# Optimization experiments

Hardware: AMD Instinct MI355X
Metric: run time of the kernel (lower is better)

Reference implementation:

```python
import jax, jax.numpy as jnp
import numpy as np

N, E, NFEAT, NHID, K, TOP_N, NCLASS = 50000, 800000, 512, 128, 4, 2, 64
ALPHA = 0.2   # LeakyReLU negative slope (config.alpha)
EPS = 1e-16   # avoid 0/0 for isolated / fully-masked nodes


def _spgat_layer(h, src, dst, a, mask, concat):
    """SpGraphAttentionLayer_2: attention over given edges, no internal W.
    h: (N, F); a: (2F,); mask: optional (E,) 0/1 edge-subset mask.
    edge_e = exp(-leakyrelu(a . [h_src; h_dst]));
    out = segsum(e * h_dst) / segsum(e)  (per target node src).
    """
    F = h.shape[1]
    s1 = h @ a[:F]                     # (N,)
    s2 = h @ a[F:]                     # (N,)
    e = jnp.exp(-jax.nn.leaky_relu(s1[src] + s2[dst], ALPHA))  # (E,)
    if mask is not None:
        e = e * mask
    rowsum = jax.ops.segment_sum(e, src, num_segments=N)              # (N,)
    hp = jax.ops.segment_sum(e[:, None] * h[dst], src, num_segments=N)  # (N,F)
    hp = hp / (rowsum[:, None] + EPS)
    return jax.nn.elu(hp) if concat else hp


def setup_inputs() -> dict:
    key = jax.random.key(0)
    ks = jax.random.split(key, 7)
    x = jax.random.normal(ks[0], (N, NFEAT), jnp.float32)
    edge = jax.random.randint(ks[1], (2, E), 0, N)
    W_ks = jax.random.normal(ks[2], (K, NFEAT, NHID), jnp.float32) * 0.05
    a_k = jax.random.normal(ks[3], (K, 2 * NHID * K), jnp.float32) * 0.05
    W_o = jax.random.normal(ks[4], (NHID * K, NCLASS), jnp.float32) * 0.05
    a_att = jax.random.normal(ks[5], (K, 2 * NHID), jnp.float32) * 0.05
    a_out = jax.random.normal(ks[6], (2 * NCLASS,), jnp.float32) * 0.05
    return {"x": x, "edge": edge, "W_ks": W_ks, "a_k": a_k,
            "W_o": W_o, "a_att": a_att, "a_out": a_out}


def reference(x, edge, W_ks, a_k, W_o, a_att, a_out):
    src, dst = edge[0], edge[1]
    # K per-factor projections; dropout is a no-op in eval mode
    h_k = jnp.einsum('nf,kfh->knh', x, W_ks)              # (K, N, H)
    h = jnp.transpose(h_k, (1, 0, 2)).reshape(N, K * NHID)  # cat(h_k, dim=1)
    # Edge-level factor routing: softmax_K( a_k @ [h_src; h_dst] ).
    # Linear score => precompute per-node halves instead of (E, 2KH) gather.
    s_src = h @ a_k[:, :K * NHID].T                       # (N, K)
    s_dst = h @ a_k[:, K * NHID:].T                       # (N, K)
    edge_att = jax.nn.softmax(s_src[src] + s_dst[dst], axis=-1)  # (E, K)
    top_att, top_idx = jax.lax.top_k(edge_att, TOP_N)     # (E, TOP_N)
    # edge e belongs to factor k iff k is among its top_n factors
    masks = (top_idx[:, :, None] == jnp.arange(K)[None, None, :]).any(1)  # (E, K)
    outs = [_spgat_layer(h_k[k], src, dst, a_att[k],
                         masks[:, k].astype(h.dtype), True) for k in range(K)]
    xo = jnp.concatenate(outs, axis=1) @ W_o              # (N, NCLASS)
    xo = jax.nn.elu(_spgat_layer(xo, src, dst, a_out, None, False))
    att_loss = jnp.mean(1.0 - jnp.sum(top_att, axis=1))
    return jax.nn.log_softmax(xo, axis=1), att_loss
```

## Files before the change

kernel.cpp:

```cpp
#include <hip/hip_runtime.h>
#include <math.h>

#define NN 50000
#define NE 800000
#define NF 512
#define NH 128
#define KF 4
#define NC 64
#define LRELU_ALPHA 0.2f
#define EPSF 1e-16f

typedef unsigned short u16;
typedef __attribute__((ext_vector_type(8))) short bf16x8;
typedef __attribute__((ext_vector_type(4))) float f32x4;

#define OFF_H      0LL
#define OFF_HP     (OFF_H + (long long)NN * NF)
#define OFF_REC    (OFF_HP + (long long)NN * NF)
#define OFF_XO0    (OFF_REC + 4LL * NE)
#define OFF_SV1    (OFF_XO0 + (long long)NN * NC)
#define OFF_SV2    (OFF_SV1 + (long long)NN * 8)
#define OFF_WOT    (OFF_SV2 + (long long)NN * 8)
#define OFF_S1O    (OFF_WOT + (long long)NN * KF)
#define OFF_S2O    (OFF_S1O + NN)
#define OFF_START  (OFF_S2O + NN)
#define OFF_CNT    (OFF_START + NN + 4)
#define OFF_CURSOR (OFF_CNT + NN)
#define OFF_ATT    (OFF_CURSOR + NN)
#define WS_FLOATS  (OFF_ATT + 2)

__device__ __forceinline__ u16 bf16_rne(float f) {
    unsigned int u = __float_as_uint(f);
    return (u16)((u + 0x7FFFu + ((u >> 16) & 1u)) >> 16);
}
__device__ __forceinline__ float bf16_f(u16 b) {
    return __uint_as_float(((unsigned int)b) << 16);
}

__device__ __forceinline__ void gload_lds16(const u16* g, u16* l) {
    __builtin_amdgcn_global_load_lds(
        (const __attribute__((address_space(1))) void*)g,
        (__attribute__((address_space(3))) void*)l, 16, 0, 0);
}

#define NSPLIT 12500
#define NCNT   ((NE + 255) / 256)
__global__ __launch_bounds__(256) void split_all(
        const float* __restrict__ x, u16* __restrict__ xhi, u16* __restrict__ xlo,
        const int* __restrict__ edge, int* __restrict__ cnt,
        const float* __restrict__ Wks, const float* __restrict__ Wo,
        u16* __restrict__ wthi, u16* __restrict__ wtlo,
        u16* __restrict__ wohi, u16* __restrict__ wolo) {
    if (blockIdx.x < NSPLIT) {
        size_t i = ((size_t)blockIdx.x * 256 + threadIdx.x) * 8;
        float4 v0 = *(const float4*)(x + i);
        float4 v1 = *(const float4*)(x + i + 4);
        float v[8] = {v0.x, v0.y, v0.z, v0.w, v1.x, v1.y, v1.z, v1.w};
        unsigned int hp[4], lp[4];
#pragma unroll
        for (int j = 0; j < 4; ++j) {
            u16 h0 = bf16_rne(v[2 * j]);
            u16 h1 = bf16_rne(v[2 * j + 1]);
            u16 l0 = bf16_rne(v[2 * j] - bf16_f(h0));
            u16 l1 = bf16_rne(v[2 * j + 1] - bf16_f(h1));
            hp[j] = (unsigned int)h0 | ((unsigned int)h1 << 16);
            lp[j] = (unsigned int)l0 | ((unsigned int)l1 << 16);
        }
        *(uint4*)(xhi + i) = make_uint4(hp[0], hp[1], hp[2], hp[3]);
        *(uint4*)(xlo + i) = make_uint4(lp[0], lp[1], lp[2], lp[3]);
    } else if (blockIdx.x < NSPLIT + NCNT) {
        int e = (blockIdx.x - NSPLIT) * 256 + threadIdx.x;
        if (e < NE) atomicAdd(&cnt[edge[e]], 1);
    } else {
        int b = blockIdx.x - NSPLIT - NCNT;
        if (b < 512) {
            int kf = b >> 7, n = b & 127;
            for (int f = threadIdx.x; f < NF; f += 256) {
                float v = Wks[(size_t)kf * (NF * NH) + (size_t)f * NH + n];
                u16 hb = bf16_rne(v);
                u16 lb = bf16_rne(v - bf16_f(hb));
                wthi[(size_t)b * NF + f] = hb;
                wtlo[(size_t)b * NF + f] = lb;
            }
        } else {
            int n = b - 512;
            for (int f = threadIdx.x; f < NF; f += 256) {
                float v = Wo[(size_t)f * NC + n];
                u16 hb = bf16_rne(v);
                u16 lb = bf16_rne(v - bf16_f(hb));
                wohi[(size_t)n * NF + f] = hb;
                wolo[(size_t)n * NF + f] = lb;
            }
        }
    }
}

__global__ __launch_bounds__(256) void gemm_h_mfma(
        const u16* __restrict__ xhi, const u16* __restrict__ xlo,
        const u16* __restrict__ wthi, const u16* __restrict__ wtlo,
        float* __restrict__ h) {
    __shared__ u16 Ah[128 * 32], Al[128 * 32], Bh[128 * 32], Bl[128 * 32];
    const int nwg = 4 * ((NN + 127) / 128);
    const int q = nwg / 8, r = nwg % 8;
    int o = blockIdx.x;
    int xcd = o & 7, pos = o >> 3;
    int wg = (xcd < r ? xcd * (q + 1) : r * (q + 1) + (xcd - r) * q) + pos;
    int m0 = (wg >> 2) * 128, n0 = (wg & 3) * 128;

    int tid = threadIdx.x;
    int lane = tid & 63;
    int wave = tid >> 6, wm = wave >> 1, wn = wave & 1;
    f32x4 acc[4][4];
#pragma unroll
    for (int i = 0; i < 4; ++i)
#pragma unroll
        for (int j = 0; j < 4; ++j) acc[i][j] = (f32x4)(0.f);

    u16* sbuf = (wave == 0) ? Ah : (wave == 1) ? Al : (wave == 2) ? Bh : Bl;
    const u16* gbase = (wave == 0) ? xhi : (wave == 1) ? xlo
                     : (wave == 2) ? wthi : wtlo;
    int rowbase = (wave < 2) ? m0 : n0;
    int c16s = (lane & 3) ^ ((lane >> 2) & 3) ^ (lane >> 4);
    const u16* gsrc[8];
#pragma unroll
    for (int i = 0; i < 8; ++i) {
        int rowg = rowbase + 16 * i + (lane >> 2);
        if (wave < 2 && rowg >= NN) rowg = NN - 1;
        gsrc[i] = gbase + (size_t)rowg * NF + c16s * 8;
    }

    const int arow = wm * 64 + (lane & 15);
    const int brow = wn * 64 + (lane & 15);
    const int rc16 = (lane >> 4) ^ ((lane & 3) ^ ((lane >> 2) & 3));
    const int fragoff = rc16 * 8;

    for (int k0 = 0; k0 < NF; k0 += 32) {
        __syncthreads();
#pragma unroll
        for (int i = 0; i < 8; ++i)
            gload_lds16(gsrc[i] + k0, sbuf + i * 512);
        __syncthreads();
        bf16x8 ah[4], al[4], bh[4], bl[4];
#pragma unroll
        for (int mi = 0; mi < 4; ++mi) {
            ah[mi] = *(const bf16x8*)(Ah + (arow + mi * 16) * 32 + fragoff);
            al[mi] = *(const bf16x8*)(Al + (arow + mi * 16) * 32 + fragoff);
        }
#pragma unroll
        for (int ni = 0; ni < 4; ++ni) {
            bh[ni] = *(const bf16x8*)(Bh + (brow + ni * 16) * 32 + fragoff);
            bl[ni] = *(const bf16x8*)(Bl + (brow + ni * 16) * 32 + fragoff);
        }
#pragma unroll
        for (int mi = 0; mi < 4; ++mi)
#pragma unroll
            for (int ni = 0; ni < 4; ++ni) {
                acc[mi][ni] = __builtin_amdgcn_mfma_f32_16x16x32_bf16(
                    ah[mi], bh[ni], acc[mi][ni], 0, 0, 0);
                acc[mi][ni] = __builtin_amdgcn_mfma_f32_16x16x32_bf16(
                    ah[mi], bl[ni], acc[mi][ni], 0, 0, 0);
                acc[mi][ni] = __builtin_amdgcn_mfma_f32_16x16x32_bf16(
                    al[mi], bh[ni], acc[mi][ni], 0, 0, 0);
            }
    }
#pragma unroll
    for (int mi = 0; mi < 4; ++mi) {
        int mbase = m0 + wm * 64 + mi * 16 + (lane >> 4) * 4;
#pragma unroll
        for (int ni = 0; ni < 4; ++ni) {
            int n = n0 + wn * 64 + ni * 16 + (lane & 15);
#pragma unroll
            for (int r2 = 0; r2 < 4; ++r2) {
                int m = mbase + r2;
                if (m < NN) h[(size_t)m * NF + n] = acc[mi][ni][r2];
            }
        }
    }
}

__global__ __launch_bounds__(256) void compute_svals_h(
        const float* __restrict__ h, const float* __restrict__ a_k,
        const float* __restrict__ a_att,
        float* __restrict__ sv1, float* __restrict__ sv2) {
    __shared__ float Ak[4][1024];
    __shared__ float Aa[4][256];
    for (int i = threadIdx.x; i < 4096; i += 256) Ak[i >> 10][i & 1023] = a_k[i];
    for (int i = threadIdx.x; i < 1024; i += 256) Aa[i >> 8][i & 255] = a_att[i];
    __syncthreads();
    int w = threadIdx.x >> 6, lane = threadIdx.x & 63;
    for (int n = blockIdx.x * 4 + w; n < NN; n += gridDim.x * 4) {
        const float* hr = h + (size_t)n * NF;
        float accS[4] = {0, 0, 0, 0}, accD[4] = {0, 0, 0, 0};
        float accQ1[4] = {0, 0, 0, 0}, accQ2[4] = {0, 0, 0, 0};
#pragma unroll
        for (int i = 0; i < 8; ++i) {
            int f = i * 64 + lane;
            float hv = hr[f];
#pragma unroll
            for (int k = 0; k < 4; ++k) {
                accS[k] = fmaf(hv, Ak[k][f], accS[k]);
                accD[k] = fmaf(hv, Ak[k][512 + f], accD[k]);
            }
            accQ1[i >> 1] = fmaf(hv, Aa[i >> 1][f & 127], accQ1[i >> 1]);
            accQ2[i >> 1] = fmaf(hv, Aa[i >> 1][128 + (f & 127)], accQ2[i >> 1]);
        }
#pragma unroll
        for (int off = 32; off >= 1; off >>= 1) {
#pragma unroll
            for (int k = 0; k < 4; ++k) {
                accS[k] += __shfl_xor(accS[k], off);
                accD[k] += __shfl_xor(accD[k], off);
                accQ1[k] += __shfl_xor(accQ1[k], off);
                accQ2[k] += __shfl_xor(accQ2[k], off);
            }
        }
        if (lane == 0) {
#pragma unroll
            for (int k = 0; k < 4; ++k) {
                sv1[(size_t)n * 8 + k]     = accS[k];
                sv1[(size_t)n * 8 + 4 + k] = accQ1[k];
                sv2[(size_t)n * 8 + k]     = accD[k];
                sv2[(size_t)n * 8 + 4 + k] = accQ2[k];
            }
        }
    }
}

__global__ __launch_bounds__(1024) void csr_scan(const int* __restrict__ cnt,
                                                 int* __restrict__ start) {
    __shared__ int part[1024];
    int t = threadIdx.x;
    const int CH = (NN + 1023) / 1024;
    int base = t * CH;
    int s = 0;
    for (int i = 0; i < CH; ++i) {
        int idx = base + i;
        if (idx < NN) s += cnt[idx];
    }
    part[t] = s;
    __syncthreads();
    for (int off = 1; off < 1024; off <<= 1) {
        int v = (t >= off) ? part[t - off] : 0;
        __syncthreads();
        part[t] += v;
        __syncthreads();
    }
    int run = (t == 0) ? 0 : part[t - 1];
    for (int i = 0; i < CH; ++i) {
        int idx = base + i;
        if (idx < NN) { start[idx] = run; run += cnt[idx]; }
    }
    if (t == 1023) start[NN] = run;
}

__global__ __launch_bounds__(256) void edge_pre1(
        const int* __restrict__ edge, const int* __restrict__ start,
        int* __restrict__ cursor,
        const float* __restrict__ sv1, const float* __restrict__ sv2,
        int4* __restrict__ rec, double* __restrict__ att_acc) {
    __shared__ float blk[4];
    int tid = threadIdx.x;
    int e = blockIdx.x * 256 + tid;
    float t2 = 0.f;
    if (e < NE) {
        int src = edge[e];
        int dst = edge[NE + e];
        const float* p1 = sv1 + (size_t)src * 8;
        const float* p2 = sv2 + (size_t)dst * 8;
        float4 ss = *(const float4*)(p1);
        float4 q1 = *(const float4*)(p1 + 4);
        float4 sd = *(const float4*)(p2);
        float4 q2 = *(const float4*)(p2 + 4);
        float l0 = ss.x + sd.x, l1 = ss.y + sd.y, l2 = ss.z + sd.z, l3 = ss.w + sd.w;
        int i1 = 0; float v1 = l0;
        if (l1 > v1) { v1 = l1; i1 = 1; }
        if (l2 > v1) { v1 = l2; i1 = 2; }
        if (l3 > v1) { v1 = l3; i1 = 3; }
        int i2 = 0; float v2 = -3.4e38f;
        if (i1 != 0)            { v2 = l0; i2 = 0; }
        if (i1 != 1 && l1 > v2) { v2 = l1; i2 = 1; }
        if (i1 != 2 && l2 > v2) { v2 = l2; i2 = 2; }
        if (i1 != 3 && l3 > v2) { v2 = l3; i2 = 3; }
        float esum = expf(l0 - v1) + expf(l1 - v1) + expf(l2 - v1) + expf(l3 - v1);
        t2 = (1.f + expf(v2 - v1)) / esum;
        float q1v1 = i1 == 0 ? q1.x : i1 == 1 ? q1.y : i1 == 2 ? q1.z : q1.w;
        float q2v1 = i1 == 0 ? q2.x : i1 == 1 ? q2.y : i1 == 2 ? q2.z : q2.w;
        float q1v2 = i2 == 0 ? q1.x : i2 == 1 ? q1.y : i2 == 2 ? q1.z : q1.w;
        float q2v2 = i2 == 0 ? q2.x : i2 == 1 ? q2.y : i2 == 2 ? q2.z : q2.w;
        float sv1v = q1v1 + q2v1, sv2v = q1v2 + q2v2;
        float ee1 = expf(-(sv1v >= 0.f ? sv1v : LRELU_ALPHA * sv1v));
        float ee2 = expf(-(sv2v >= 0.f ? sv2v : LRELU_ALPHA * sv2v));
        int p = start[src] + atomicAdd(&cursor[src], 1);
        rec[p] = make_int4(dst, src | (i1 << 16) | (i2 << 18),
                           __float_as_int(ee1), __float_as_int(ee2));
    }
#pragma unroll
    for (int off = 32; off >= 1; off >>= 1) t2 += __shfl_xor(t2, off);
    if ((tid & 63) == 0) blk[tid >> 6] = t2;
    __syncthreads();
    if (tid == 0)
        atomicAdd(att_acc, (double)(blk[0] + blk[1] + blk[2] + blk[3]));
}

#define G1_LOAD(RR, T)                                                          \
    int i1##T = __builtin_amdgcn_readfirstlane(((RR).y >> 16) & 3);             \
    int i2##T = __builtin_amdgcn_readfirstlane(((RR).y >> 18) & 3);             \
    int dd##T = __builtin_amdgcn_readfirstlane((RR).x);                         \
    float w1##T = __uint_as_float(__builtin_amdgcn_readfirstlane((RR).z));      \
    float w2##T = __uint_as_float(__builtin_amdgcn_readfirstlane((RR).w));      \
    const float* hr##T = h + (size_t)dd##T * NF + lane;                         \
    float v1a##T = hr##T[i1##T * 128];                                          \
    float v1b##T = hr##T[i1##T * 128 + 64];                                     \
    float v2a##T = hr##T[i2##T * 128];                                          \
    float v2b##T = hr##T[i2##T * 128 + 64];

#define G1_ACC(T)                                                               \
    switch (i1##T) {                                                            \
        case 0: a00 = fmaf(w1##T, v1a##T, a00); a01 = fmaf(w1##T, v1b##T, a01); rs0 += w1##T; break; \
        case 1: a10 = fmaf(w1##T, v1a##T, a10); a11 = fmaf(w1##T, v1b##T, a11); rs1 += w1##T; break; \
        case 2: a20 = fmaf(w1##T, v1a##T, a20); a21 = fmaf(w1##T, v1b##T, a21); rs2 += w1##T; break; \
        default:a30 = fmaf(w1##T, v1a##T, a30); a31 = fmaf(w1##T, v1b##T, a31); rs3 += w1##T; break; \
    }                                                                           \
    switch (i2##T) {                                                            \
        case 0: a00 = fmaf(w2##T, v2a##T, a00); a01 = fmaf(w2##T, v2b##T, a01); rs0 += w2##T; break; \
        case 1: a10 = fmaf(w2##T, v2a##T, a10); a11 = fmaf(w2##T, v2b##T, a11); rs1 += w2##T; break; \
        case 2: a20 = fmaf(w2##T, v2a##T, a20); a21 = fmaf(w2##T, v2b##T, a21); rs2 += w2##T; break; \
        default:a30 = fmaf(w2##T, v2a##T, a30); a31 = fmaf(w2##T, v2b##T, a31); rs3 += w2##T; break; \
    }

__global__ __launch_bounds__(256) void node_gather1(
        const int* __restrict__ start, const int4* __restrict__ rec,
        const float* __restrict__ h,
        u16* __restrict__ ahi, u16* __restrict__ alo) {
    __shared__ float red[4][512];
    __shared__ float rsred[4][4];
    int n = blockIdx.x;
    int w = threadIdx.x >> 6, lane = threadIdx.x & 63;
    int j0 = __builtin_amdgcn_readfirstlane(start[n]);
    int j1 = __builtin_amdgcn_readfirstlane(start[n + 1]);
    float a00 = 0.f, a01 = 0.f, a10 = 0.f, a11 = 0.f;
    float a20 = 0.f, a21 = 0.f, a30 = 0.f, a31 = 0.f;
    float rs0 = 0.f, rs1 = 0.f, rs2 = 0.f, rs3 = 0.f;
    int j = j0 + w;
    for (; j + 12 < j1; j += 16) {
        int4 r0 = rec[j];
        int4 r1 = rec[j + 4];
        int4 r2 = rec[j + 8];
        int4 r3 = rec[j + 12];
        G1_LOAD(r0, A) G1_LOAD(r1, B) G1_LOAD(r2, C) G1_LOAD(r3, D)
        G1_ACC(A) G1_ACC(B) G1_ACC(C) G1_ACC(D)
    }
    for (; j < j1; j += 4) {
        int4 r0 = rec[j];
        G1_LOAD(r0, A)
        G1_ACC(A)
    }
    red[w][lane]       = a00; red[w][64 + lane]  = a01;
    red[w][128 + lane] = a10; red[w][192 + lane] = a11;
    red[w][256 + lane] = a20; red[w][320 + lane] = a21;
    red[w][384 + lane] = a30; red[w][448 + lane] = a31;
    if (lane == 0) {
        rsred[w][0] = rs0; rsred[w][1] = rs1; rsred[w][2] = rs2; rsred[w][3] = rs3;
    }
    __syncthreads();
    int t = threadIdx.x;
    float s0 = (red[0][t] + red[1][t]) + (red[2][t] + red[3][t]);
    float s1 = (red[0][256 + t] + red[1][256 + t]) + (red[2][256 + t] + red[3][256 + t]);
    int f0 = t >> 7, f1 = 2 + (t >> 7);
    float rsa = (rsred[0][f0] + rsred[1][f0]) + (rsred[2][f0] + rsred[3][f0]) + EPSF;
    float rsb = (rsred[0][f1] + rsred[1][f1]) + (rsred[2][f1] + rsred[3][f1]) + EPSF;
    float e0 = s0 / rsa; e0 = e0 > 0.f ? e0 : expm1f(e0);
    float e1 = s1 / rsb; e1 = e1 > 0.f ? e1 : expm1f(e1);
    u16 h0 = bf16_rne(e0), l0 = bf16_rne(e0 - bf16_f(h0));
    u16 h1 = bf16_rne(e1), l1 = bf16_rne(e1 - bf16_f(h1));
    u16* ah = ahi + (size_t)n * NF;
    u16* al = alo + (size_t)n * NF;
    ah[t] = h0; ah[256 + t] = h1;
    al[t] = l0; al[256 + t] = l1;
}

__global__ __launch_bounds__(256) void node_pass_mfma(
        const u16* __restrict__ ahi, const u16* __restrict__ alo,
        const u16* __restrict__ wohi, const u16* __restrict__ wolo,
        const float* __restrict__ a_out,
        float* __restrict__ xo0, float* __restrict__ s1o, float* __restrict__ s2o) {
    __shared__ u16 Ah[128 * 32], Al[128 * 32], Bh[64 * 32], Bl[64 * 32];
    __shared__ float part1[2][64][2];
    __shared__ float part2[2][64][2];
    int m0 = blockIdx.x * 128;
    int tid = threadIdx.x;
    int lane = tid & 63;
    int wave = tid >> 6, wm = wave >> 1, wn = wave & 1;
    f32x4 acc[4][2];
#pragma unroll
    for (int i = 0; i < 4; ++i)
#pragma unroll
        for (int j = 0; j < 2; ++j) acc[i][j] = (f32x4)(0.f);

    u16* sbuf = (wave == 0) ? Ah : (wave == 1) ? Al : (wave == 2) ? Bh : Bl;
    const u16* gbase = (wave == 0) ? ahi : (wave == 1) ? alo
                     : (wave == 2) ? wohi : wolo;
    int nld = (wave < 2) ? 8 : 4;
    int c16s = (lane & 3) ^ ((lane >> 2) & 3) ^ (lane >> 4);
    const u16* gsrc[8];
#pragma unroll
    for (int i = 0; i < 8; ++i) {
        int rowg = ((wave < 2) ? m0 : 0) + 16 * i + (lane >> 2);
        if (wave < 2 && rowg >= NN) rowg = NN - 1;
        gsrc[i] = gbase + (size_t)rowg * NF + c16s * 8;
    }

    const int arow = wm * 64 + (lane & 15);
    const int brow = wn * 32 + (lane & 15);
    const int rc16 = (lane >> 4) ^ ((lane & 3) ^ ((lane >> 2) & 3));
    const int fragoff = rc16 * 8;

    for (int k0 = 0; k0 < NF; k0 += 32) {
        __syncthreads();
        for (int i = 0; i < nld; ++i)
            gload_lds16(gsrc[i] + k0, sbuf + i * 512);
        __syncthreads();
        bf16x8 ah[4], al[4], bh[2], bl[2];
#pragma unroll
        for (int mi = 0; mi < 4; ++mi) {
            ah[mi] = *(const bf16x8*)(Ah + (arow + mi * 16) * 32 + fragoff);
            al[mi] = *(const bf16x8*)(Al + (arow + mi * 16) * 32 + fragoff);
        }
#pragma unroll
        for (int ni = 0; ni < 2; ++ni) {
            bh[ni] = *(const bf16x8*)(Bh + (brow + ni * 16) * 32 + fragoff);
            bl[ni] = *(const bf16x8*)(Bl + (brow + ni * 16) * 32 + fragoff);
        }
#pragma unroll
        for (int mi = 0; mi < 4; ++mi)
#pragma unroll
            for (int ni = 0; ni < 2; ++ni) {
                acc[mi][ni] = __builtin_amdgcn_mfma_f32_16x16x32_bf16(
                    ah[mi], bh[ni], acc[mi][ni], 0, 0, 0);
                acc[mi][ni] = __builtin_amdgcn_mfma_f32_16x16x32_bf16(
                    ah[mi], bl[ni], acc[mi][ni], 0, 0, 0);
                acc[mi][ni] = __builtin_amdgcn_mfma_f32_16x16x32_bf16(
                    al[mi], bh[ni], acc[mi][ni], 0, 0, 0);
            }
    }
#pragma unroll
    for (int mi = 0; mi < 4; ++mi) {
        int mbase = m0 + wm * 64 + mi * 16 + (lane >> 4) * 4;
#pragma unroll
        for (int ni = 0; ni < 2; ++ni) {
            int n = wn * 32 + ni * 16 + (lane & 15);
#pragma unroll
            for (int r2 = 0; r2 < 4; ++r2) {
                int m = mbase + r2;
                if (m < NN) xo0[(size_t)m * NC + n] = acc[mi][ni][r2];
            }
        }
    }
    float ao1[2], ao2[2];
#pragma unroll
    for (int ni = 0; ni < 2; ++ni) {
        int c = wn * 32 + ni * 16 + (lane & 15);
        ao1[ni] = a_out[c];
        ao2[ni] = a_out[64 + c];
    }
#pragma unroll
    for (int mi = 0; mi < 4; ++mi)
#pragma unroll
        for (int r2 = 0; r2 < 4; ++r2) {
            float p1 = acc[mi][0][r2] * ao1[0] + acc[mi][1][r2] * ao1[1];
            float p2 = acc[mi][0][r2] * ao2[0] + acc[mi][1][r2] * ao2[1];
#pragma unroll
            for (int off = 8; off >= 1; off >>= 1) {
                p1 += __shfl_xor(p1, off);
                p2 += __shfl_xor(p2, off);
            }
            if ((lane & 15) == 0) {
                int rl = mi * 16 + (lane >> 4) * 4 + r2;
                part1[wm][rl][wn] = p1;
                part2[wm][rl][wn] = p2;
            }
        }
    __syncthreads();
    if (tid < 128) {
        int m = m0 + tid;
        if (m < NN) {
            s1o[m] = part1[tid >> 6][tid & 63][0] + part1[tid >> 6][tid & 63][1];
            s2o[m] = part2[tid >> 6][tid & 63][0] + part2[tid >> 6][tid & 63][1];
        }
    }
}

__global__ __launch_bounds__(256) void node_gather2(
        const int* __restrict__ start, const int4* __restrict__ rec,
        const float* __restrict__ s1o, const float* __restrict__ s2o,
        const float* __restrict__ xo0, const double* __restrict__ att_acc,
        float* __restrict__ out) {
    __shared__ float red[4][64];
    __shared__ float rsl[4];
    if (blockIdx.x == 0 && threadIdx.x == 0)
        out[(size_t)NN * NC] = 1.f - (float)(att_acc[0] / (double)NE);
    int n = blockIdx.x;
    int w = threadIdx.x >> 6, lane = threadIdx.x & 63;
    int j0 = __builtin_amdgcn_readfirstlane(start[n]);
    int j1 = __builtin_amdgcn_readfirstlane(start[n + 1]);
    float s1n = s1o[n];
    float acc = 0.f, rsum = 0.f;
    int j = j0 + w;
    for (; j + 12 < j1; j += 16) {
        int d0 = __builtin_amdgcn_readfirstlane(rec[j].x);
        int d1 = __builtin_amdgcn_readfirstlane(rec[j + 4].x);
        int d2 = __builtin_amdgcn_readfirstlane(rec[j + 8].x);
        int d3 = __builtin_amdgcn_readfirstlane(rec[j + 12].x);
        float t0 = s1n + s2o[d0];
        float t1 = s1n + s2o[d1];
        float t2 = s1n + s2o[d2];
        float t3 = s1n + s2o[d3];
        float x0 = xo0[(size_t)d0 * NC + lane];
        float x1 = xo0[(size_t)d1 * NC + lane];
        float x2 = xo0[(size_t)d2 * NC + lane];
        float x3 = xo0[(size_t)d3 * NC + lane];
        float e0 = expf(-(t0 >= 0.f ? t0 : LRELU_ALPHA * t0));
        float e1 = expf(-(t1 >= 0.f ? t1 : LRELU_ALPHA * t1));
        float e2 = expf(-(t2 >= 0.f ? t2 : LRELU_ALPHA * t2));
        float e3 = expf(-(t3 >= 0.f ? t3 : LRELU_ALPHA * t3));
        acc = fmaf(e0, x0, acc); rsum += e0;
        acc = fmaf(e1, x1, acc); rsum += e1;
        acc = fmaf(e2, x2, acc); rsum += e2;
        acc = fmaf(e3, x3, acc); rsum += e3;
    }
    for (; j < j1; j += 4) {
        int d = __builtin_amdgcn_readfirstlane(rec[j].x);
        float sv = s1n + s2o[d];
        float e = expf(-(sv >= 0.f ? sv : LRELU_ALPHA * sv));
        acc = fmaf(e, xo0[(size_t)d * NC + lane], acc);
        rsum += e;
    }
    red[w][lane] = acc;
    if (lane == 0) rsl[w] = rsum;
    __syncthreads();
    if (w == 0) {
        float a = (red[0][lane] + red[1][lane]) + (red[2][lane] + red[3][lane]);
        float r = (rsl[0] + rsl[1]) + (rsl[2] + rsl[3]);
        float t = a / (r + EPSF);
        float v = t > 0.f ? t : expm1f(t);
        float m = v;
#pragma unroll
        for (int off = 32; off >= 1; off >>= 1) m = fmaxf(m, __shfl_xor(m, off));
        float p = expf(v - m);
#pragma unroll
        for (int off = 32; off >= 1; off >>= 1) p += __shfl_xor(p, off);
        out[(size_t)n * NC + lane] = v - m - logf(p);
    }
}

extern "C" void kernel_launch(void* const* d_in, const int* in_sizes, int n_in,
                              void* d_out, int out_size, void* d_ws, size_t ws_size,
                              hipStream_t stream) {
    const float* x     = (const float*)d_in[0];
    const int*   edge  = (const int*)d_in[1];
    const float* Wks   = (const float*)d_in[2];
    const float* a_k   = (const float*)d_in[3];
    const float* Wo    = (const float*)d_in[4];
    const float* a_att = (const float*)d_in[5];
    const float* a_out = (const float*)d_in[6];
    float* out = (float*)d_out;

    float* wsf = (float*)d_ws;
    float* h      = wsf + OFF_H;
    int4*  rec    = (int4*)(wsf + OFF_REC);
    float* xo0    = wsf + OFF_XO0;
    float* sv1    = wsf + OFF_SV1;
    float* sv2    = wsf + OFF_SV2;
    float* s1o    = wsf + OFF_S1O;
    float* s2o    = wsf + OFF_S2O;
    int*   startp = (int*)(wsf + OFF_START);
    int*   cnt    = (int*)(wsf + OFF_CNT);
    int*   cursor = (int*)(wsf + OFF_CURSOR);
    double* att   = (double*)(wsf + OFF_ATT);

    u16* xhi  = (u16*)(wsf + OFF_HP);
    u16* xlo  = xhi + (size_t)NN * NF;
    u16* ahi  = xhi;
    u16* alo  = xlo;
    u16* wthi = (u16*)(wsf + OFF_REC);
    u16* wtlo = wthi + (size_t)KF * NH * NF;
    u16* wohi = (u16*)(wsf + OFF_WOT);
    u16* wolo = wohi + (size_t)NC * NF;

    size_t zero_bytes = (size_t)(WS_FLOATS - OFF_CNT) * sizeof(float);
    hipMemsetAsync((char*)d_ws + (size_t)OFF_CNT * sizeof(float), 0, zero_bytes, stream);

    split_all<<<NSPLIT + NCNT + 576, 256, 0, stream>>>(
        x, xhi, xlo, edge, cnt, Wks, Wo, wthi, wtlo, wohi, wolo);
    csr_scan<<<1, 1024, 0, stream>>>(cnt, startp);
    gemm_h_mfma<<<4 * ((NN + 127) / 128), 256, 0, stream>>>(xhi, xlo, wthi, wtlo, h);
    compute_svals_h<<<2048, 256, 0, stream>>>(h, a_k, a_att, sv1, sv2);
    edge_pre1<<<(NE + 255) / 256, 256, 0, stream>>>(edge, startp, cursor,
                                                    sv1, sv2, rec, att);
    node_gather1<<<NN, 256, 0, stream>>>(startp, rec, h, ahi, alo);
    node_pass_mfma<<<(NN + 127) / 128, 256, 0, stream>>>(ahi, alo, wohi, wolo,
                                                         a_out, xo0, s1o, s2o);
    node_gather2<<<NN, 256, 0, stream>>>(startp, rec, s1o, s2o, xo0, att, out);
}
```

Baseline: 586.3 us.

## Double-buffer LDS in h GEMM and precompute output-layer edge weights

The projection GEMM now uses two LDS buffers, so global-to-LDS loads for the next K-slice are issued while MFMAs run on the current one. This removes one barrier per iteration at the cost of doubled shared memory, which may lower occupancy. Separately, a new per-edge kernel computes the output-layer attention weights (exp of leaky-relu scores) into a workspace array. The final gather then reads those weights instead of doing the s2o gather and exp per node block, at the cost of an extra launch and an extra array read.

```diff
diff --git a/kernel.cpp b/kernel.cpp
--- a/kernel.cpp
+++ b/kernel.cpp
@@ -24,7 +24,8 @@
 #define OFF_S1O    (OFF_WOT + (long long)NN * KF)
 #define OFF_S2O    (OFF_S1O + NN)
 #define OFF_START  (OFF_S2O + NN)
-#define OFF_CNT    (OFF_START + NN + 4)
+#define OFF_EEO    (OFF_START + NN + 4)
+#define OFF_CNT    (OFF_EEO + NE)
 #define OFF_CURSOR (OFF_CNT + NN)
 #define OFF_ATT    (OFF_CURSOR + NN)
 #define WS_FLOATS  (OFF_ATT + 2)
@@ -99,7 +100,7 @@
         const u16* __restrict__ xhi, const u16* __restrict__ xlo,
         const u16* __restrict__ wthi, const u16* __restrict__ wtlo,
         float* __restrict__ h) {
-    __shared__ u16 Ah[128 * 32], Al[128 * 32], Bh[128 * 32], Bl[128 * 32];
+    __shared__ u16 S[2][4][128 * 32];
     const int nwg = 4 * ((NN + 127) / 128);
     const int q = nwg / 8, r = nwg % 8;
     int o = blockIdx.x;
@@ -116,7 +117,6 @@
 #pragma unroll
         for (int j = 0; j < 4; ++j) acc[i][j] = (f32x4)(0.f);
 
-    u16* sbuf = (wave == 0) ? Ah : (wave == 1) ? Al : (wave == 2) ? Bh : Bl;
     const u16* gbase = (wave == 0) ? xhi : (wave == 1) ? xlo
                      : (wave == 2) ? wthi : wtlo;
     int rowbase = (wave < 2) ? m0 : n0;
@@ -128,28 +128,42 @@
         if (wave < 2 && rowg >= NN) rowg = NN - 1;
         gsrc[i] = gbase + (size_t)rowg * NF + c16s * 8;
     }
+    u16* dst0 = &S[0][wave][0];
+    u16* dst1 = &S[1][wave][0];
 
     const int arow = wm * 64 + (lane & 15);
     const int brow = wn * 64 + (lane & 15);
     const int rc16 = (lane >> 4) ^ ((lane & 3) ^ ((lane >> 2) & 3));
     const int fragoff = rc16 * 8;
 
-    for (int k0 = 0; k0 < NF; k0 += 32) {
-        __syncthreads();
-#pragma unroll
-        for (int i = 0; i < 8; ++i)
-            gload_lds16(gsrc[i] + k0, sbuf + i * 512);
-        __syncthreads();
+#pragma unroll
+    for (int i = 0; i < 8; ++i)
+        gload_lds16(gsrc[i], dst0 + i * 512);
+    __syncthreads();
+
+    for (int t = 0; t < 16; ++t) {
+        int cur = t & 1;
+        if (t + 1 < 16) {
+            u16* nd = cur ? dst0 : dst1;
+            int k0n = (t + 1) * 32;
+#pragma unroll
+            for (int i = 0; i < 8; ++i)
+                gload_lds16(gsrc[i] + k0n, nd + i * 512);
+        }
+        const u16* Ah_ = &S[cur][0][0];
+        const u16* Al_ = &S[cur][1][0];
+        const u16* Bh_ = &S[cur][2][0];
+        const u16* Bl_ = &S[cur][3][0];
         bf16x8 ah[4], al[4], bh[4], bl[4];
 #pragma unroll
         for (int mi = 0; mi < 4; ++mi) {
-            ah[mi] = *(const bf16x8*)(Ah + (arow + mi * 16) * 32 + fragoff);
-            al[mi] = *(const bf16x8*)(Al + (arow + mi * 16) * 32 + fragoff);
+            ah[mi] = *(const bf16x8*)(Ah_ + (arow + mi * 16) * 32 + fragoff);
+            al[mi] = *(const bf16x8*)(Al_ + (arow + mi * 16) * 32 + fragoff);
         }
 #pragma unroll
         for (int ni = 0; ni < 4; ++ni) {
-            bh[ni] = *(const bf16x8*)(Bh + (brow + ni * 16) * 32 + fragoff);
-            bl[ni] = *(const bf16x8*)(Bl + (brow + ni * 16) * 32 + fragoff);
+            bh[ni] = *(const bf16x8*)(Bh_ + (brow + ni * 16) * 32 + fragoff);
+            bl[ni] = *(const bf16x8*)(Bl_ + (brow + ni * 16) * 32 + fragoff);
         }
 #pragma unroll
         for (int mi = 0; mi < 4; ++mi)
@@ -162,6 +176,7 @@
                 acc[mi][ni] = __builtin_amdgcn_mfma_f32_16x16x32_bf16(
                     al[mi], bh[ni], acc[mi][ni], 0, 0, 0);
             }
+        __syncthreads();
     }
 #pragma unroll
     for (int mi = 0; mi < 4; ++mi) {
@@ -490,11 +505,21 @@
     }
 }
 
+__global__ __launch_bounds__(256) void edge_ee2(
+        const int4* __restrict__ rec, const float* __restrict__ s1o,
+        const float* __restrict__ s2o, float* __restrict__ eeo) {
+    int p = blockIdx.x * 256 + threadIdx.x;
+    if (p >= NE) return;
+    int4 r = rec[p];
+    int src = r.y & 0xFFFF;
+    float sv = s1o[src] + s2o[r.x];
+    eeo[p] = expf(-(sv >= 0.f ? sv : LRELU_ALPHA * sv));
+}
+
 __global__ __launch_bounds__(256) void node_gather2(
         const int* __restrict__ start, const int4* __restrict__ rec,
-        const float* __restrict__ s1o, const float* __restrict__ s2o,
-        const float* __restrict__ xo0, const double* __restrict__ att_acc,
-        float* __restrict__ out) {
+        const float* __restrict__ eeo, const float* __restrict__ xo0,
+        const double* __restrict__ att_acc, float* __restrict__ out) {
     __shared__ float red[4][64];
     __shared__ float rsl[4];
     if (blockIdx.x == 0 && threadIdx.x == 0)
@@ -503,35 +528,29 @@
     int w = threadIdx.x >> 6, lane = threadIdx.x & 63;
     int j0 = __builtin_amdgcn_readfirstlane(start[n]);
     int j1 = __builtin_amdgcn_readfirstlane(start[n + 1]);
-    float s1n = s1o[n];
     float acc = 0.f, rsum = 0.f;
     int j = j0 + w;
     for (; j + 12 < j1; j += 16) {
-        int d0 = __builtin_amdgcn_readfirstlane(rec[j].x);
-        int d1 = __builtin_amdgcn_readfirstlane(rec[j + 4].x);
-        int d2 = __builtin_amdgcn_readfirstlane(rec[j + 8].x);
-        int d3 = __builtin_amdgcn_readfirstlane(rec[j + 12].x);
-        float t0 = s1n + s2o[d0];
-        float t1 = s1n + s2o[d1];
-        float t2 = s1n + s2o[d2];
-        float t3 = s1n + s2o[d3];
+        int d0 = rec[j].x;
+        int d1 = rec[j + 4].x;
+        int d2 = rec[j + 8].x;
+        int d3 = rec[j + 12].x;
+        float e0 = eeo[j];
+        float e1 = eeo[j + 4];
+        float e2 = eeo[j + 8];
+        float e3 = eeo[j + 12];
         float x0 = xo0[(size_t)d0 * NC + lane];
         float x1 = xo0[(size_t)d1 * NC + lane];
         float x2 = xo0[(size_t)d2 * NC + lane];
         float x3 = xo0[(size_t)d3 * NC + lane];
-        float e0 = expf(-(t0 >= 0.f ? t0 : LRELU_ALPHA * t0));
-        float e1 = expf(-(t1 >= 0.f ? t1 : LRELU_ALPHA * t1));
-        float e2 = expf(-(t2 >= 0.f ? t2 : LRELU_ALPHA * t2));
-        float e3 = expf(-(t3 >= 0.f ? t3 : LRELU_ALPHA * t3));
         acc = fmaf(e0, x0, acc); rsum += e0;
         acc = fmaf(e1, x1, acc); rsum += e1;
         acc = fmaf(e2, x2, acc); rsum += e2;
         acc = fmaf(e3, x3, acc); rsum += e3;
     }
     for (; j < j1; j += 4) {
-        int d = __builtin_amdgcn_readfirstlane(rec[j].x);
-        float sv = s1n + s2o[d];
-        float e = expf(-(sv >= 0.f ? sv : LRELU_ALPHA * sv));
+        int d = rec[j].x;
+        float e = eeo[j];
         acc = fmaf(e, xo0[(size_t)d * NC + lane], acc);
         rsum += e;
     }
@@ -573,6 +592,7 @@
     float* sv2    = wsf + OFF_SV2;
     float* s1o    = wsf + OFF_S1O;
     float* s2o    = wsf + OFF_S2O;
+    float* eeo    = wsf + OFF_EEO;
     int*   startp = (int*)(wsf + OFF_START);
     int*   cnt    = (int*)(wsf + OFF_CNT);
     int*   cursor = (int*)(wsf + OFF_CURSOR);
@@ -600,5 +620,6 @@
     node_gather1<<<NN, 256, 0, stream>>>(startp, rec, h, ahi, alo);
     node_pass_mfma<<<(NN + 127) / 128, 256, 0, stream>>>(ahi, alo, wohi, wolo,
                                                          a_out, xo0, s1o, s2o);
-    node_gather2<<<NN, 256, 0, stream>>>(startp, rec, s1o, s2o, xo0, att, out);
-}
+    edge_ee2<<<(NE + 255) / 256, 256, 0, stream>>>(rec, s1o, s2o, eeo);
+    node_gather2<<<NN, 256, 0, stream>>>(startp, rec, eeo, xo0, att, out);
+}
```

Measured after the change: 589.6 us. Within noise of the previous version (+0.6%).
